# Kernel optimization log

Measured on AMD Instinct MI355X. Metric: run time of the kernel, lower is better.

Reference implementation:

```python
import jax, jax.numpy as jnp
import numpy as np

NEG_SLOPE = 0.2
EPS = 1e-16

def gat_conv(x, edge_index, W, a_src, a_dst, b):
    # x: [N, Fin], W: [Fin, C], a_src/a_dst: [C], b: [C]
    N = x.shape[0]
    src, dst = edge_index[0], edge_index[1]
    h = x @ W                                  # [N, C]
    alpha_s = h @ a_src                        # [N]
    alpha_d = h @ a_dst                        # [N]
    e = alpha_s[src] + alpha_d[dst]            # [E]
    e = jnp.where(e > 0, e, NEG_SLOPE * e)     # LeakyReLU(0.2)
    # ragged softmax over incoming edges of each dst node
    m = jax.ops.segment_max(e, dst, num_segments=N)       # [N]
    p = jnp.exp(e - m[dst])                                # [E]
    s = jax.ops.segment_sum(p, dst, num_segments=N)        # [N]
    alpha = p / (s[dst] + EPS)                             # [E]
    out = jax.ops.segment_sum(alpha[:, None] * h[src], dst, num_segments=N)
    return out + b

def setup_inputs() -> dict:
    key = jax.random.key(0)
    ks = jax.random.split(key, 10)
    N, Fin, H, C, E = 50000, 128, 64, 64, 800000
    x = jax.random.normal(ks[0], (N, Fin), dtype=jnp.float32)
    edge_index = jax.random.randint(ks[1], (2, E), 0, N, dtype=jnp.int64)
    sc1 = 1.0 / np.sqrt(Fin)
    sc2 = 1.0 / np.sqrt(H)
    W1 = jax.random.normal(ks[2], (Fin, H), dtype=jnp.float32) * sc1
    a_src1 = jax.random.normal(ks[3], (H,), dtype=jnp.float32) * sc2
    a_dst1 = jax.random.normal(ks[4], (H,), dtype=jnp.float32) * sc2
    b1 = jnp.zeros((H,), dtype=jnp.float32)
    W2 = jax.random.normal(ks[5], (H, C), dtype=jnp.float32) * sc2
    a_src2 = jax.random.normal(ks[6], (C,), dtype=jnp.float32) * sc2
    a_dst2 = jax.random.normal(ks[7], (C,), dtype=jnp.float32) * sc2
    b2 = jnp.zeros((C,), dtype=jnp.float32)
    return {"x": x, "edge_index": edge_index, "W1": W1, "a_src1": a_src1,
            "a_dst1": a_dst1, "b1": b1, "W2": W2, "a_src2": a_src2,
            "a_dst2": a_dst2, "b2": b2}

def reference(x, edge_index, W1, a_src1, a_dst1, b1, W2, a_src2, a_dst2, b2):
    h = gat_conv(x, edge_index, W1, a_src1, a_dst1, b1)
    h = jax.nn.relu(h)
    out = gat_conv(h, edge_index, W2, a_src2, a_dst2, b2)
    return out
```

## Files before the change

kernel.cpp:

```cpp
#include <hip/hip_runtime.h>
#include <cstddef>

constexpr int FIN = 128;
constexpr int EPB = 2048;
constexpr int BSH = 7;
constexpr int NPB = 128;
constexpr int PACK_SH = 25;

typedef _Float16 half4 __attribute__((ext_vector_type(4)));
typedef _Float16 half8 __attribute__((ext_vector_type(8)));
typedef float floatx4 __attribute__((ext_vector_type(4)));

__device__ __forceinline__ int block_scan_tot(int v, int tid, int* wsums,
                                              int* tot) {
    int lane = tid & 63, w = tid >> 6;
    int x = v;
#pragma unroll
    for (int off = 1; off < 64; off <<= 1) {
        int y = __shfl_up(x, off, 64);
        if (lane >= off) x += y;
    }
    if (lane == 63) wsums[w] = x;
    __syncthreads();
    int add = 0;
#pragma unroll
    for (int i = 0; i < 4; ++i) add += (i < w) ? wsums[i] : 0;
    *tot = wsums[0] + wsums[1] + wsums[2] + wsums[3];
    return x + add - v;
}

template <int K, typename XT>
__device__ __forceinline__
void gemm_mfma_body(const XT* __restrict__ X, const float* __restrict__ W,
                    const float* __restrict__ ASRC, const float* __restrict__ ADST,
                    _Float16* __restrict__ Hh, float* __restrict__ AS,
                    float* __restrict__ AD, int N, int blk,
                    _Float16* Xh, _Float16* WT) {
    constexpr int LDH = K + 8;
    const int tid = threadIdx.x;
    const int nb = blk * 64;

    if constexpr (sizeof(XT) == 4) {
        constexpr int QPR = K / 4;
        for (int i = tid; i < 64 * QPR; i += 256) {
            int r = i / QPR, q = i % QPR;
            float4 v = make_float4(0.f, 0.f, 0.f, 0.f);
            if (nb + r < N) v = *(const float4*)(X + (size_t)(nb + r) * K + 4 * q);
            half4 h; h[0] = (_Float16)v.x; h[1] = (_Float16)v.y;
            h[2] = (_Float16)v.z; h[3] = (_Float16)v.w;
            *(half4*)(Xh + r * LDH + 4 * q) = h;
        }
    } else {
        constexpr int OPR = K / 8;
        for (int i = tid; i < 64 * OPR; i += 256) {
            int r = i / OPR, o = i % OPR;
            half8 v = {};
            if (nb + r < N) v = *(const half8*)(X + (size_t)(nb + r) * K + 8 * o);
            *(half8*)(Xh + r * LDH + 8 * o) = v;
        }
    }
    for (int i = tid; i < 64 * (K / 4); i += 256) {
        int n = i & 63, kg = i >> 6;
        half4 h;
#pragma unroll
        for (int j = 0; j < 4; ++j)
            h[j] = (_Float16)W[(4 * kg + j) * 64 + n];
        *(half4*)(WT + n * LDH + 4 * kg) = h;
    }
    __syncthreads();

    const int l = tid & 63;
    const int r0 = (tid >> 6) * 16;
    const int n16 = l & 15, quad = l >> 4;

    floatx4 acc[4];
#pragma unroll
    for (int nt = 0; nt < 4; ++nt) acc[nt] = (floatx4){0.f, 0.f, 0.f, 0.f};

#pragma unroll
    for (int k0 = 0; k0 < K; k0 += 32) {
        half8 a = *(const half8*)(Xh + (r0 + n16) * LDH + k0 + quad * 8);
#pragma unroll
        for (int nt = 0; nt < 4; ++nt) {
            half8 b = *(const half8*)(WT + (nt * 16 + n16) * LDH + k0 + quad * 8);
            acc[nt] = __builtin_amdgcn_mfma_f32_16x16x32_f16(a, b, acc[nt], 0, 0, 0);
        }
    }

    float pa[4] = {0.f, 0.f, 0.f, 0.f}, pd[4] = {0.f, 0.f, 0.f, 0.f};
#pragma unroll
    for (int nt = 0; nt < 4; ++nt) {
        float as_v = ASRC[nt * 16 + n16], ad_v = ADST[nt * 16 + n16];
#pragma unroll
        for (int reg = 0; reg < 4; ++reg) {
            pa[reg] += acc[nt][reg] * as_v;
            pd[reg] += acc[nt][reg] * ad_v;
        }
    }
#pragma unroll
    for (int off = 1; off < 16; off <<= 1) {
#pragma unroll
        for (int reg = 0; reg < 4; ++reg) {
            pa[reg] += __shfl_xor(pa[reg], off, 64);
            pd[reg] += __shfl_xor(pd[reg], off, 64);
        }
    }
    if (n16 == 0) {
#pragma unroll
        for (int reg = 0; reg < 4; ++reg) {
            int row = nb + r0 + quad * 4 + reg;
            if (row < N) { AS[row] = pa[reg]; AD[row] = pd[reg]; }
        }
    }

#pragma unroll
    for (int nt = 0; nt < 4; ++nt)
#pragma unroll
        for (int reg = 0; reg < 4; ++reg)
            Xh[(r0 + quad * 4 + reg) * LDH + nt * 16 + n16] = (_Float16)acc[nt][reg];
    {
        int r = r0 + (l >> 2);
        int o = (l & 3) * 16;
        if (nb + r < N) {
            half8 v0 = *(const half8*)(Xh + r * LDH + o);
            half8 v1 = *(const half8*)(Xh + r * LDH + o + 8);
            *(half8*)(Hh + (size_t)(nb + r) * 64 + o) = v0;
            *(half8*)(Hh + (size_t)(nb + r) * 64 + o + 8) = v1;
        }
    }
}

__global__ __launch_bounds__(256)
void gemm1_and_count(const float* __restrict__ X, const float* __restrict__ W,
                     const float* __restrict__ ASRC, const float* __restrict__ ADST,
                     _Float16* __restrict__ Hh, float* __restrict__ AS,
                     float* __restrict__ AD, int N,
                     const int* __restrict__ dst, int E, int nblk, int nbuck,
                     int* __restrict__ cnts, int* __restrict__ ticket) {
    constexpr int K = FIN, LDH = K + 8;
    __shared__ _Float16 Xh[64 * LDH];
    __shared__ _Float16 WT[64 * LDH];

    const int tid = threadIdx.x;
    if ((int)blockIdx.x < nblk) {
        int* hist = (int*)Xh;
        if (blockIdx.x == 0 && tid == 0) *ticket = 0;
        for (int i = tid; i < nbuck; i += 256) hist[i] = 0;
        __syncthreads();
        int e0 = blockIdx.x * EPB;
        int e1 = min(e0 + EPB, E);
        for (int e = e0 + tid; e < e1; e += 256)
            atomicAdd(&hist[dst[e] >> BSH], 1);
        __syncthreads();
        for (int i = tid; i < nbuck; i += 256)
            cnts[blockIdx.x * nbuck + i] = hist[i];
        return;
    }
    gemm_mfma_body<K, float>(X, W, ASRC, ADST, Hh, AS, AD, N,
                             blockIdx.x - nblk, Xh, WT);
}

template <int K, typename XT>
__global__ __launch_bounds__(256)
void gemm_feat(const XT* __restrict__ X, const float* __restrict__ W,
               const float* __restrict__ ASRC, const float* __restrict__ ADST,
               _Float16* __restrict__ Hh, float* __restrict__ AS,
               float* __restrict__ AD, int N) {
    constexpr int LDH = K + 8;
    __shared__ _Float16 Xh[64 * LDH];
    __shared__ _Float16 WT[64 * LDH];
    gemm_mfma_body<K, XT>(X, W, ASRC, ADST, Hh, AS, AD, N, blockIdx.x, Xh, WT);
}

__global__ __launch_bounds__(256)
void bucket_colscan_fused(int* __restrict__ cnts, int nblk, int nbuck,
                          int* __restrict__ btotal, int* __restrict__ bbase,
                          int* __restrict__ ticket) {
    __shared__ int wsums[4];
    __shared__ int lastflag;
    int b = blockIdx.x;
    int tid = threadIdx.x;
    int carry = 0;
    for (int c0 = 0; c0 < nblk; c0 += 256) {
        int t = c0 + tid;
        int v = (t < nblk) ? cnts[t * nbuck + b] : 0;
        int tot;
        int e = block_scan_tot(v, tid, wsums, &tot);
        if (t < nblk) cnts[t * nbuck + b] = e + carry;
        carry += tot;
        __syncthreads();
    }
    if (tid == 0) {
        atomicExch(&btotal[b], carry);
        int old = atomicAdd(ticket, 1);
        lastflag = (old == nbuck - 1);
    }
    __syncthreads();
    if (!lastflag) return;
    int i0 = 2 * tid, i1 = 2 * tid + 1;
    int v0 = (i0 < nbuck) ? atomicAdd(&btotal[i0], 0) : 0;
    int v1 = (i1 < nbuck) ? atomicAdd(&btotal[i1], 0) : 0;
    __syncthreads();
    int tot2;
    int e2 = block_scan_tot(v0 + v1, tid, wsums, &tot2);
    if (i0 <= nbuck) bbase[i0] = e2;
    if (i1 <= nbuck) bbase[i1] = e2 + v0;
}

__global__ __launch_bounds__(256)
void bucket_scatter(const int* __restrict__ src, const int* __restrict__ dst,
                    int E, int nbuck, const int* __restrict__ cnts,
                    const int* __restrict__ bbase, int* __restrict__ ebuck) {
    __shared__ int cur[512];
    int tid = threadIdx.x;
    for (int i = tid; i < nbuck; i += 256)
        cur[i] = bbase[i] + cnts[blockIdx.x * nbuck + i];
    __syncthreads();
    int e0 = blockIdx.x * EPB;
    int e1 = min(e0 + EPB, E);
    for (int e = e0 + tid; e < e1; e += 256) {
        int d = dst[e];
        int p = atomicAdd(&cur[d >> BSH], 1);
        ebuck[p] = ((d & (NPB - 1)) << PACK_SH) | src[e];
    }
}

__global__ __launch_bounds__(256)
void bucket_to_csr(const int* __restrict__ ebuck, const int* __restrict__ bbase,
                   int N, int E, int* __restrict__ row_ptr,
                   int* __restrict__ csr_src) {
    __shared__ int hist[NPB];
    __shared__ int cur[NPB];
    __shared__ int wsums[4];
    int b = blockIdx.x, tid = threadIdx.x;
    int nstart = b << BSH;
    int base = bbase[b], endp = bbase[b + 1];
    if (tid < NPB) hist[tid] = 0;
    __syncthreads();
    for (int e = base + tid; e < endp; e += 256)
        atomicAdd(&hist[((unsigned)ebuck[e]) >> PACK_SH], 1);
    __syncthreads();
    int v = (tid < NPB) ? hist[tid] : 0;
    int tot;
    int excl = block_scan_tot(v, tid, wsums, &tot);
    if (tid < NPB) {
        cur[tid] = excl;
        if (nstart + tid < N) row_ptr[nstart + tid] = base + excl;
    }
    if (b == 0 && tid == 0) row_ptr[N] = E;
    __syncthreads();
    for (int e = base + tid; e < endp; e += 256) {
        int pv = ebuck[e];
        int p = atomicAdd(&cur[((unsigned)pv) >> PACK_SH], 1);
        csr_src[base + p] = pv & ((1 << PACK_SH) - 1);
    }
}

template <typename OT>
__device__ __forceinline__
void agg_one_node(const _Float16* __restrict__ Hh, const float* __restrict__ AS,
                  const float* __restrict__ AD, const int* __restrict__ csr_src,
                  const float* __restrict__ bias, OT* __restrict__ OUT,
                  int n, int base, int end, int lane, int relu) {
    const int cnt = end - base;
    const float adn = AD[n];

    if (cnt > 64) {
        float m = -INFINITY;
        for (int c0 = base; c0 < end; c0 += 64) {
            int c = min(64, end - c0);
            float e = -INFINITY;
            if (lane < c) {
                int sr = csr_src[c0 + lane];
                float t = AS[sr] + adn;
                e = t > 0.f ? t : 0.2f * t;
            }
#pragma unroll
            for (int off = 32; off > 0; off >>= 1) e = fmaxf(e, __shfl_xor(e, off, 64));
            m = fmaxf(m, e);
        }
        float s = 0.f, acc = 0.f;
        for (int c0 = base; c0 < end; c0 += 64) {
            int c = min(64, end - c0);
            int srcl = 0;
            float p = 0.f;
            if (lane < c) {
                srcl = csr_src[c0 + lane];
                float t = AS[srcl] + adn;
                t = t > 0.f ? t : 0.2f * t;
                p = __expf(t - m);
            }
            float cs = p;
#pragma unroll
            for (int off = 32; off > 0; off >>= 1) cs += __shfl_xor(cs, off, 64);
            s += cs;
            for (int j = 0; j < c; ++j)
                acc += __shfl(p, j, 64) *
                       (float)Hh[(size_t)__shfl(srcl, j, 64) * 64 + lane];
        }
        float o = acc * (1.f / (s + 1e-16f)) + bias[lane];
        if (relu) o = fmaxf(o, 0.f);
        OUT[(size_t)n * 64 + lane] = (OT)o;
        return;
    }

    int srcl = 0;
    float el = 0.f;
    if (lane < cnt) {
        srcl = csr_src[base + lane];
        float e = AS[srcl] + adn;
        el = e > 0.f ? e : 0.2f * e;
    }
    float p = (lane < cnt) ? __expf(el) : 0.f;
    float s = p;
#pragma unroll
    for (int off = 32; off > 0; off >>= 1) s += __shfl_xor(s, off, 64);
    const float inv = 1.f / (s + 1e-16f);

    const int eg = lane >> 3;
    const int c8 = (lane & 7) * 8;

    float acc[8], acc2[8];
#pragma unroll
    for (int t = 0; t < 8; ++t) { acc[t] = 0.f; acc2[t] = 0.f; }

    int j = 0;
    for (; j + 16 <= cnt; j += 16) {
        int iA = j + eg, iB = j + 8 + eg;
        int sA = __shfl(srcl, iA, 64), sB = __shfl(srcl, iB, 64);
        float aA = __shfl(p, iA, 64),  aB = __shfl(p, iB, 64);
        half8 hA = *(const half8*)(Hh + (size_t)sA * 64 + c8);
        half8 hB = *(const half8*)(Hh + (size_t)sB * 64 + c8);
#pragma unroll
        for (int t = 0; t < 8; ++t) {
            acc[t]  += aA * (float)hA[t];
            acc2[t] += aB * (float)hB[t];
        }
    }
    for (; j < cnt; j += 8) {
        int iA = j + eg;
        int sA = __shfl(srcl, iA, 64);
        float aA = __shfl(p, iA, 64);
        half8 hA = *(const half8*)(Hh + (size_t)sA * 64 + c8);
#pragma unroll
        for (int t = 0; t < 8; ++t) acc[t] += aA * (float)hA[t];
    }
#pragma unroll
    for (int t = 0; t < 8; ++t) acc[t] += acc2[t];
#pragma unroll
    for (int off = 8; off <= 32; off <<= 1)
#pragma unroll
        for (int t = 0; t < 8; ++t) acc[t] += __shfl_xor(acc[t], off, 64);

    if (lane < 8) {
        float4 b0 = *(const float4*)(bias + c8);
        float4 b1 = *(const float4*)(bias + c8 + 4);
        float o[8];
        o[0] = acc[0] * inv + b0.x; o[1] = acc[1] * inv + b0.y;
        o[2] = acc[2] * inv + b0.z; o[3] = acc[3] * inv + b0.w;
        o[4] = acc[4] * inv + b1.x; o[5] = acc[5] * inv + b1.y;
        o[6] = acc[6] * inv + b1.z; o[7] = acc[7] * inv + b1.w;
        if (relu) {
#pragma unroll
            for (int t = 0; t < 8; ++t) o[t] = fmaxf(o[t], 0.f);
        }
        if constexpr (sizeof(OT) == 2) {
            half8 hv;
#pragma unroll
            for (int t = 0; t < 8; ++t) hv[t] = (_Float16)o[t];
            *(half8*)((_Float16*)OUT + (size_t)n * 64 + c8) = hv;
        } else {
            *(float4*)((float*)OUT + (size_t)n * 64 + c8) =
                make_float4(o[0], o[1], o[2], o[3]);
            *(float4*)((float*)OUT + (size_t)n * 64 + c8 + 4) =
                make_float4(o[4], o[5], o[6], o[7]);
        }
    }
}

template <typename OT>
__global__ __launch_bounds__(256)
void gat_aggregate(const _Float16* __restrict__ Hh, const float* __restrict__ AS,
                   const float* __restrict__ AD, const int* __restrict__ row_ptr,
                   const int* __restrict__ csr_src, const float* __restrict__ bias,
                   OT* __restrict__ OUT, int N, int relu) {
    const int lane = threadIdx.x & 63;
    const int half = lane >> 5;
    const int l32  = lane & 31;
    const int pair0 = blockIdx.x * 8 + (threadIdx.x >> 6) * 2;
    if (pair0 >= N) return;
    const int n = pair0 + half;

    int base = 0, end = 0;
    if (n < N) { base = row_ptr[n]; end = row_ptr[n + 1]; }
    const int cnt = end - base;

    if (!__all(cnt <= 32)) {
        int baseA = __shfl(base, 0, 64),  endA = __shfl(end, 0, 64);
        int baseB = __shfl(base, 32, 64), endB = __shfl(end, 32, 64);
        agg_one_node(Hh, AS, AD, csr_src, bias, OUT, pair0, baseA, endA, lane, relu);
        if (pair0 + 1 < N)
            agg_one_node(Hh, AS, AD, csr_src, bias, OUT, pair0 + 1, baseB, endB,
                         lane, relu);
        return;
    }

    const float adn = (n < N) ? AD[n] : 0.f;
    int srcl = 0;
    float p = 0.f;
    if (l32 < cnt) {
        srcl = csr_src[base + l32];
        float e = AS[srcl] + adn;
        e = e > 0.f ? e : 0.2f * e;
        p = __expf(e);
    }
    float s = p;
#pragma unroll
    for (int off = 16; off > 0; off >>= 1) s += __shfl_xor(s, off, 64);
    const float inv = 1.f / (s + 1e-16f);

    const int eg = l32 >> 3;
    const int c8 = (l32 & 7) * 8;

    float acc[8], acc2[8];
#pragma unroll
    for (int t = 0; t < 8; ++t) { acc[t] = 0.f; acc2[t] = 0.f; }

    int j = 0;
    for (; j + 8 <= cnt; j += 8) {
        int iA = j + eg, iB = j + 4 + eg;
        int sA = __shfl(srcl, iA, 32), sB = __shfl(srcl, iB, 32);
        float aA = __shfl(p, iA, 32),  aB = __shfl(p, iB, 32);
        half8 hA = *(const half8*)(Hh + (size_t)sA * 64 + c8);
        half8 hB = *(const half8*)(Hh + (size_t)sB * 64 + c8);
#pragma unroll
        for (int t = 0; t < 8; ++t) {
            acc[t]  += aA * (float)hA[t];
            acc2[t] += aB * (float)hB[t];
        }
    }
    for (; j < cnt; j += 4) {
        int iA = j + eg;
        int sA = __shfl(srcl, iA, 32);
        float aA = __shfl(p, iA, 32);
        half8 hA = *(const half8*)(Hh + (size_t)sA * 64 + c8);
#pragma unroll
        for (int t = 0; t < 8; ++t) acc[t] += aA * (float)hA[t];
    }
#pragma unroll
    for (int t = 0; t < 8; ++t) acc[t] += acc2[t];
#pragma unroll
    for (int t = 0; t < 8; ++t) acc[t] += __shfl_xor(acc[t], 8, 64);
#pragma unroll
    for (int t = 0; t < 8; ++t) acc[t] += __shfl_xor(acc[t], 16, 64);

    if (l32 < 8 && n < N) {
        float4 b0 = *(const float4*)(bias + c8);
        float4 b1 = *(const float4*)(bias + c8 + 4);
        float o[8];
        o[0] = acc[0] * inv + b0.x; o[1] = acc[1] * inv + b0.y;
        o[2] = acc[2] * inv + b0.z; o[3] = acc[3] * inv + b0.w;
        o[4] = acc[4] * inv + b1.x; o[5] = acc[5] * inv + b1.y;
        o[6] = acc[6] * inv + b1.z; o[7] = acc[7] * inv + b1.w;
        if (relu) {
#pragma unroll
            for (int t = 0; t < 8; ++t) o[t] = fmaxf(o[t], 0.f);
        }
        if constexpr (sizeof(OT) == 2) {
            half8 hv;
#pragma unroll
            for (int t = 0; t < 8; ++t) hv[t] = (_Float16)o[t];
            *(half8*)((_Float16*)OUT + (size_t)n * 64 + c8) = hv;
        } else {
            *(float4*)((float*)OUT + (size_t)n * 64 + c8) =
                make_float4(o[0], o[1], o[2], o[3]);
            *(float4*)((float*)OUT + (size_t)n * 64 + c8 + 4) =
                make_float4(o[4], o[5], o[6], o[7]);
        }
    }
}

extern "C" void kernel_launch(void* const* d_in, const int* in_sizes, int n_in,
                              void* d_out, int out_size, void* d_ws, size_t ws_size,
                              hipStream_t stream) {
    const float* x    = (const float*)d_in[0];
    const int*   ei   = (const int*)d_in[1];
    const float* W1   = (const float*)d_in[2];
    const float* as1w = (const float*)d_in[3];
    const float* ad1w = (const float*)d_in[4];
    const float* b1   = (const float*)d_in[5];
    const float* W2   = (const float*)d_in[6];
    const float* as2w = (const float*)d_in[7];
    const float* ad2w = (const float*)d_in[8];
    const float* b2   = (const float*)d_in[9];
    float* out = (float*)d_out;

    const int N = in_sizes[0] / FIN;
    const int E = in_sizes[1] / 2;
    const int* esrc = ei;
    const int* edst = ei + E;

    const int nbuck = (N + NPB - 1) >> BSH;
    const int nblk  = (E + EPB - 1) / EPB;

    char* wp8 = (char*)d_ws;
    _Float16* Hh  = (_Float16*)wp8;  wp8 += (size_t)N * 64 * 2;
    _Float16* R1h = (_Float16*)wp8;  wp8 += (size_t)N * 64 * 2;
    float* AS1 = (float*)wp8;        wp8 += (size_t)N * 4;
    float* AD1 = (float*)wp8;        wp8 += (size_t)N * 4;
    float* AS2 = (float*)wp8;        wp8 += (size_t)N * 4;
    float* AD2 = (float*)wp8;        wp8 += (size_t)N * 4;
    int* row_ptr = (int*)wp8;        wp8 += (size_t)(N + 1) * 4;
    int* csr     = (int*)wp8;        wp8 += (size_t)E * 4;
    int* ebuck   = (int*)wp8;        wp8 += (size_t)E * 4;
    int* cnts    = (int*)wp8;        wp8 += (size_t)nblk * nbuck * 4;
    int* btotal  = (int*)wp8;        wp8 += (size_t)nbuck * 4;
    int* bbase   = (int*)wp8;        wp8 += (size_t)(nbuck + 1) * 4;
    int* ticket  = (int*)wp8;        wp8 += 4;

    const int nbG = (N + 63) / 64;
    const int nbAgg = (N + 7) / 8;

    hipLaunchKernelGGL(gemm1_and_count, dim3(nblk + nbG), dim3(256), 0, stream,
                       x, W1, as1w, ad1w, Hh, AS1, AD1, N,
                       edst, E, nblk, nbuck, cnts, ticket);
    hipLaunchKernelGGL(bucket_colscan_fused, dim3(nbuck), dim3(256), 0, stream,
                       cnts, nblk, nbuck, btotal, bbase, ticket);
    hipLaunchKernelGGL(bucket_scatter, dim3(nblk), dim3(256), 0, stream,
                       esrc, edst, E, nbuck, cnts, bbase, ebuck);
    hipLaunchKernelGGL(bucket_to_csr, dim3(nbuck), dim3(256), 0, stream,
                       ebuck, bbase, N, E, row_ptr, csr);
    hipLaunchKernelGGL(gat_aggregate<_Float16>, dim3(nbAgg), dim3(256), 0,
                       stream, Hh, AS1, AD1, row_ptr, csr, b1, R1h, N, 1);
    hipLaunchKernelGGL((gemm_feat<64, _Float16>), dim3(nbG), dim3(256), 0, stream,
                       R1h, W2, as2w, ad2w, Hh, AS2, AD2, N);
    hipLaunchKernelGGL(gat_aggregate<float>, dim3(nbAgg), dim3(256), 0,
                       stream, Hh, AS2, AD2, row_ptr, csr, b2, out, N, 0);
}
```

Before: 174.7 us.

## Build CSR via per-node degree atomics instead of two-pass bucket sort

Replaces the bucketed counting sort (per-block bucket histograms, column scan, bucket scatter, then per-bucket CSR build) with a direct global per-node degree count, a per-bucket scan of degrees, and a single scatter using per-node global atomic cursors. This removes one kernel launch and the intermediate packed edge buffer pass, and adds a memset. The cost moves to 800k global atomics on degree and cursor arrays, and the edge order within each row becomes nondeterministic, which may change floating-point sums and locality.

```diff
diff --git a/kernel.cpp b/kernel.cpp
--- a/kernel.cpp
+++ b/kernel.cpp
@@ -5,7 +5,6 @@
 constexpr int EPB = 2048;
 constexpr int BSH = 7;
 constexpr int NPB = 128;
-constexpr int PACK_SH = 25;
 
 typedef _Float16 half4 __attribute__((ext_vector_type(4)));
 typedef _Float16 half8 __attribute__((ext_vector_type(8)));
@@ -135,25 +134,19 @@
                      const float* __restrict__ ASRC, const float* __restrict__ ADST,
                      _Float16* __restrict__ Hh, float* __restrict__ AS,
                      float* __restrict__ AD, int N,
-                     const int* __restrict__ dst, int E, int nblk, int nbuck,
-                     int* __restrict__ cnts, int* __restrict__ ticket) {
+                     const int* __restrict__ dst, int E, int nblk,
+                     int* __restrict__ degree, int* __restrict__ ticket) {
     constexpr int K = FIN, LDH = K + 8;
     __shared__ _Float16 Xh[64 * LDH];
     __shared__ _Float16 WT[64 * LDH];
 
     const int tid = threadIdx.x;
     if ((int)blockIdx.x < nblk) {
-        int* hist = (int*)Xh;
         if (blockIdx.x == 0 && tid == 0) *ticket = 0;
-        for (int i = tid; i < nbuck; i += 256) hist[i] = 0;
-        __syncthreads();
         int e0 = blockIdx.x * EPB;
         int e1 = min(e0 + EPB, E);
         for (int e = e0 + tid; e < e1; e += 256)
-            atomicAdd(&hist[dst[e] >> BSH], 1);
-        __syncthreads();
-        for (int i = tid; i < nbuck; i += 256)
-            cnts[blockIdx.x * nbuck + i] = hist[i];
+            atomicAdd(&degree[dst[e]], 1);
         return;
     }
     gemm_mfma_body<K, float>(X, W, ASRC, ADST, Hh, AS, AD, N,
@@ -173,25 +166,21 @@
 }
 
 __global__ __launch_bounds__(256)
-void bucket_colscan_fused(int* __restrict__ cnts, int nblk, int nbuck,
-                          int* __restrict__ btotal, int* __restrict__ bbase,
-                          int* __restrict__ ticket) {
+void degree_scan(const int* __restrict__ degree, int N, int nbuck,
+                 int* __restrict__ rel, int* __restrict__ cursor,
+                 int* __restrict__ btotal, int* __restrict__ bbase,
+                 int* __restrict__ ticket) {
     __shared__ int wsums[4];
     __shared__ int lastflag;
-    int b = blockIdx.x;
-    int tid = threadIdx.x;
-    int carry = 0;
-    for (int c0 = 0; c0 < nblk; c0 += 256) {
-        int t = c0 + tid;
-        int v = (t < nblk) ? cnts[t * nbuck + b] : 0;
-        int tot;
-        int e = block_scan_tot(v, tid, wsums, &tot);
-        if (t < nblk) cnts[t * nbuck + b] = e + carry;
-        carry += tot;
-        __syncthreads();
-    }
+    int b = blockIdx.x, tid = threadIdx.x;
+    int n = (b << BSH) + tid;
+    int v = (tid < NPB && n < N) ? degree[n] : 0;
+    int tot;
+    int e = block_scan_tot(v, tid, wsums, &tot);
+    if (tid < NPB && n < N) { rel[n] = e; cursor[n] = e; }
+    __syncthreads();
     if (tid == 0) {
-        atomicExch(&btotal[b], carry);
+        atomicExch(&btotal[b], tot);
         int old = atomicAdd(ticket, 1);
         lastflag = (old == nbuck - 1);
     }
@@ -208,51 +197,20 @@
 }
 
 __global__ __launch_bounds__(256)
-void bucket_scatter(const int* __restrict__ src, const int* __restrict__ dst,
-                    int E, int nbuck, const int* __restrict__ cnts,
-                    const int* __restrict__ bbase, int* __restrict__ ebuck) {
-    __shared__ int cur[512];
+void scatter_csr(const int* __restrict__ src, const int* __restrict__ dst,
+                 int E, int N, const int* __restrict__ bbase,
+                 const int* __restrict__ rel, int* __restrict__ cursor,
+                 int* __restrict__ row_ptr, int* __restrict__ csr_src) {
     int tid = threadIdx.x;
-    for (int i = tid; i < nbuck; i += 256)
-        cur[i] = bbase[i] + cnts[blockIdx.x * nbuck + i];
-    __syncthreads();
+    for (int n = blockIdx.x * 256 + tid; n < N; n += gridDim.x * 256)
+        row_ptr[n] = bbase[n >> BSH] + rel[n];
+    if (blockIdx.x == 0 && tid == 0) row_ptr[N] = E;
     int e0 = blockIdx.x * EPB;
     int e1 = min(e0 + EPB, E);
     for (int e = e0 + tid; e < e1; e += 256) {
         int d = dst[e];
-        int p = atomicAdd(&cur[d >> BSH], 1);
-        ebuck[p] = ((d & (NPB - 1)) << PACK_SH) | src[e];
-    }
-}
-
-__global__ __launch_bounds__(256)
-void bucket_to_csr(const int* __restrict__ ebuck, const int* __restrict__ bbase,
-                   int N, int E, int* __restrict__ row_ptr,
-                   int* __restrict__ csr_src) {
-    __shared__ int hist[NPB];
-    __shared__ int cur[NPB];
-    __shared__ int wsums[4];
-    int b = blockIdx.x, tid = threadIdx.x;
-    int nstart = b << BSH;
-    int base = bbase[b], endp = bbase[b + 1];
-    if (tid < NPB) hist[tid] = 0;
-    __syncthreads();
-    for (int e = base + tid; e < endp; e += 256)
-        atomicAdd(&hist[((unsigned)ebuck[e]) >> PACK_SH], 1);
-    __syncthreads();
-    int v = (tid < NPB) ? hist[tid] : 0;
-    int tot;
-    int excl = block_scan_tot(v, tid, wsums, &tot);
-    if (tid < NPB) {
-        cur[tid] = excl;
-        if (nstart + tid < N) row_ptr[nstart + tid] = base + excl;
-    }
-    if (b == 0 && tid == 0) row_ptr[N] = E;
-    __syncthreads();
-    for (int e = base + tid; e < endp; e += 256) {
-        int pv = ebuck[e];
-        int p = atomicAdd(&cur[((unsigned)pv) >> PACK_SH], 1);
-        csr_src[base + p] = pv & ((1 << PACK_SH) - 1);
+        int p = bbase[d >> BSH] + atomicAdd(&cursor[d], 1);
+        csr_src[p] = src[e];
     }
 }
 
@@ -512,8 +470,9 @@
     float* AD2 = (float*)wp8;        wp8 += (size_t)N * 4;
     int* row_ptr = (int*)wp8;        wp8 += (size_t)(N + 1) * 4;
     int* csr     = (int*)wp8;        wp8 += (size_t)E * 4;
-    int* ebuck   = (int*)wp8;        wp8 += (size_t)E * 4;
-    int* cnts    = (int*)wp8;        wp8 += (size_t)nblk * nbuck * 4;
+    int* degree  = (int*)wp8;        wp8 += (size_t)N * 4;
+    int* rel     = (int*)wp8;        wp8 += (size_t)N * 4;
+    int* cursor  = (int*)wp8;        wp8 += (size_t)N * 4;
     int* btotal  = (int*)wp8;        wp8 += (size_t)nbuck * 4;
     int* bbase   = (int*)wp8;        wp8 += (size_t)(nbuck + 1) * 4;
     int* ticket  = (int*)wp8;        wp8 += 4;
@@ -521,15 +480,14 @@
     const int nbG = (N + 63) / 64;
     const int nbAgg = (N + 7) / 8;
 
+    hipMemsetAsync(degree, 0, (size_t)N * 4, stream);
     hipLaunchKernelGGL(gemm1_and_count, dim3(nblk + nbG), dim3(256), 0, stream,
                        x, W1, as1w, ad1w, Hh, AS1, AD1, N,
-                       edst, E, nblk, nbuck, cnts, ticket);
-    hipLaunchKernelGGL(bucket_colscan_fused, dim3(nbuck), dim3(256), 0, stream,
-                       cnts, nblk, nbuck, btotal, bbase, ticket);
-    hipLaunchKernelGGL(bucket_scatter, dim3(nblk), dim3(256), 0, stream,
-                       esrc, edst, E, nbuck, cnts, bbase, ebuck);
-    hipLaunchKernelGGL(bucket_to_csr, dim3(nbuck), dim3(256), 0, stream,
-                       ebuck, bbase, N, E, row_ptr, csr);
+                       edst, E, nblk, degree, ticket);
+    hipLaunchKernelGGL(degree_scan, dim3(nbuck), dim3(256), 0, stream,
+                       degree, N, nbuck, rel, cursor, btotal, bbase, ticket);
+    hipLaunchKernelGGL(scatter_csr, dim3(nblk), dim3(256), 0, stream,
+                       esrc, edst, E, N, bbase, rel, cursor, row_ptr, csr);
     hipLaunchKernelGGL(gat_aggregate<_Float16>, dim3(nbAgg), dim3(256), 0,
                        stream, Hh, AS1, AD1, row_ptr, csr, b1, R1h, N, 1);
     hipLaunchKernelGGL((gemm_feat<64, _Float16>), dim3(nbG), dim3(256), 0, stream,
```

Measured after the change: 230.9 us. +32.2%, slower.

## Sort edges locally in the count pass and gather buckets in LDS

Applied to the files above, without the earlier changes.

The histogram pass in the GEMM1 kernel now also sorts each 2048-edge chunk by bucket in shared memory. It writes the sorted chunk contiguously, along with per-block bucket row offsets. The separate bucket_scatter kernel and its scattered global atomic writes are removed. bucket_to_csr now gathers each bucket's runs from every chunk into an LDS buffer before the per-node counting sort. This saves a launch and a pass of random global writes, but adds more shared-memory use per block, serial per-thread gather loops, and a fixed LDS cap. Buckets larger than that cap would silently lose edges.

```diff
diff --git a/kernel.cpp b/kernel.cpp
--- a/kernel.cpp
+++ b/kernel.cpp
@@ -6,6 +6,8 @@
 constexpr int BSH = 7;
 constexpr int NPB = 128;
 constexpr int PACK_SH = 25;
+constexpr int RSTR = 512;
+constexpr int CAP = 4608;
 
 typedef _Float16 half4 __attribute__((ext_vector_type(4)));
 typedef _Float16 half8 __attribute__((ext_vector_type(8)));
@@ -131,29 +133,74 @@
 }
 
 __global__ __launch_bounds__(256)
-void gemm1_and_count(const float* __restrict__ X, const float* __restrict__ W,
-                     const float* __restrict__ ASRC, const float* __restrict__ ADST,
-                     _Float16* __restrict__ Hh, float* __restrict__ AS,
-                     float* __restrict__ AD, int N,
-                     const int* __restrict__ dst, int E, int nblk, int nbuck,
-                     int* __restrict__ cnts, int* __restrict__ ticket) {
+void gemm1_and_sort(const float* __restrict__ X, const float* __restrict__ W,
+                    const float* __restrict__ ASRC, const float* __restrict__ ADST,
+                    _Float16* __restrict__ Hh, float* __restrict__ AS,
+                    float* __restrict__ AD, int N,
+                    const int* __restrict__ src, const int* __restrict__ dst,
+                    int E, int nblk, int nbuck,
+                    int* __restrict__ cnts, int* __restrict__ rows,
+                    int* __restrict__ ebuck, int* __restrict__ ticket) {
     constexpr int K = FIN, LDH = K + 8;
     __shared__ _Float16 Xh[64 * LDH];
     __shared__ _Float16 WT[64 * LDH];
+    __shared__ int wsums[4];
 
     const int tid = threadIdx.x;
     if ((int)blockIdx.x < nblk) {
-        int* hist = (int*)Xh;
+        int* sorted = (int*)Xh;
+        int* hist   = (int*)WT;
+        int* cur    = hist + 512;
         if (blockIdx.x == 0 && tid == 0) *ticket = 0;
         for (int i = tid; i < nbuck; i += 256) hist[i] = 0;
         __syncthreads();
-        int e0 = blockIdx.x * EPB;
-        int e1 = min(e0 + EPB, E);
-        for (int e = e0 + tid; e < e1; e += 256)
-            atomicAdd(&hist[dst[e] >> BSH], 1);
+
+        const int e0 = blockIdx.x * EPB;
+        const int e1 = min(e0 + EPB, E);
+        const int cnt = e1 - e0;
+
+        int pay[8], bk[8];
+#pragma unroll
+        for (int k = 0; k < 8; ++k) {
+            int e = e0 + tid + k * 256;
+            bk[k] = -1; pay[k] = 0;
+            if (e < e1) {
+                int d = dst[e];
+                bk[k] = d >> BSH;
+                pay[k] = ((d & (NPB - 1)) << PACK_SH) | src[e];
+                atomicAdd(&hist[bk[k]], 1);
+            }
+        }
         __syncthreads();
-        for (int i = tid; i < nbuck; i += 256)
-            cnts[blockIdx.x * nbuck + i] = hist[i];
+
+        int i0 = 2 * tid, i1 = 2 * tid + 1;
+        int v0 = (i0 < nbuck) ? hist[i0] : 0;
+        int v1 = (i1 < nbuck) ? hist[i1] : 0;
+        int tot;
+        int ex = block_scan_tot(v0 + v1, tid, wsums, &tot);
+        if (i0 < nbuck) {
+            cur[i0] = ex;
+            rows[blockIdx.x * RSTR + i0] = ex;
+            cnts[blockIdx.x * nbuck + i0] = v0;
+        }
+        if (i1 < nbuck) {
+            cur[i1] = ex + v0;
+            rows[blockIdx.x * RSTR + i1] = ex + v0;
+            cnts[blockIdx.x * nbuck + i1] = v1;
+        }
+        if (tid == 0) rows[blockIdx.x * RSTR + nbuck] = cnt;
+        __syncthreads();
+
+#pragma unroll
+        for (int k = 0; k < 8; ++k) {
+            if (bk[k] >= 0) {
+                int p = atomicAdd(&cur[bk[k]], 1);
+                sorted[p] = pay[k];
+            }
+        }
+        __syncthreads();
+        for (int i = tid; i < cnt; i += 256)
+            ebuck[blockIdx.x * EPB + i] = sorted[i];
         return;
     }
     gemm_mfma_body<K, float>(X, W, ASRC, ADST, Hh, AS, AD, N,
@@ -208,37 +255,33 @@
 }
 
 __global__ __launch_bounds__(256)
-void bucket_scatter(const int* __restrict__ src, const int* __restrict__ dst,
-                    int E, int nbuck, const int* __restrict__ cnts,
-                    const int* __restrict__ bbase, int* __restrict__ ebuck) {
-    __shared__ int cur[512];
-    int tid = threadIdx.x;
-    for (int i = tid; i < nbuck; i += 256)
-        cur[i] = bbase[i] + cnts[blockIdx.x * nbuck + i];
-    __syncthreads();
-    int e0 = blockIdx.x * EPB;
-    int e1 = min(e0 + EPB, E);
-    for (int e = e0 + tid; e < e1; e += 256) {
-        int d = dst[e];
-        int p = atomicAdd(&cur[d >> BSH], 1);
-        ebuck[p] = ((d & (NPB - 1)) << PACK_SH) | src[e];
-    }
-}
-
-__global__ __launch_bounds__(256)
-void bucket_to_csr(const int* __restrict__ ebuck, const int* __restrict__ bbase,
-                   int N, int E, int* __restrict__ row_ptr,
-                   int* __restrict__ csr_src) {
+void bucket_to_csr(const int* __restrict__ ebuck, const int* __restrict__ rows,
+                   const int* __restrict__ cnts, const int* __restrict__ bbase,
+                   int N, int E, int nblk, int nbuck,
+                   int* __restrict__ row_ptr, int* __restrict__ csr_src) {
+    __shared__ int eL[CAP];
     __shared__ int hist[NPB];
     __shared__ int cur[NPB];
     __shared__ int wsums[4];
-    int b = blockIdx.x, tid = threadIdx.x;
-    int nstart = b << BSH;
-    int base = bbase[b], endp = bbase[b + 1];
+    const int b = blockIdx.x, tid = threadIdx.x;
+    const int nstart = b << BSH;
+    const int base = bbase[b], endp = bbase[b + 1];
+    const int btot = endp - base;
+
     if (tid < NPB) hist[tid] = 0;
-    __syncthreads();
-    for (int e = base + tid; e < endp; e += 256)
-        atomicAdd(&hist[((unsigned)ebuck[e]) >> PACK_SH], 1);
+    for (int blk = tid; blk < nblk; blk += 256) {
+        int r0 = rows[blk * RSTR + b];
+        int r1 = rows[blk * RSTR + b + 1];
+        int c0 = cnts[blk * nbuck + b];
+        for (int i = 0; i < r1 - r0; ++i) {
+            int c = c0 + i;
+            if (c < CAP) eL[c] = ebuck[blk * EPB + r0 + i];
+        }
+    }
+    __syncthreads();
+
+    for (int e = tid; e < btot; e += 256)
+        atomicAdd(&hist[((unsigned)eL[e]) >> PACK_SH], 1);
     __syncthreads();
     int v = (tid < NPB) ? hist[tid] : 0;
     int tot;
@@ -249,8 +292,8 @@
     }
     if (b == 0 && tid == 0) row_ptr[N] = E;
     __syncthreads();
-    for (int e = base + tid; e < endp; e += 256) {
-        int pv = ebuck[e];
+    for (int e = tid; e < btot; e += 256) {
+        int pv = eL[e];
         int p = atomicAdd(&cur[((unsigned)pv) >> PACK_SH], 1);
         csr_src[base + p] = pv & ((1 << PACK_SH) - 1);
     }
@@ -512,8 +555,9 @@
     float* AD2 = (float*)wp8;        wp8 += (size_t)N * 4;
     int* row_ptr = (int*)wp8;        wp8 += (size_t)(N + 1) * 4;
     int* csr     = (int*)wp8;        wp8 += (size_t)E * 4;
-    int* ebuck   = (int*)wp8;        wp8 += (size_t)E * 4;
+    int* ebuck   = (int*)wp8;        wp8 += (size_t)nblk * EPB * 4;
     int* cnts    = (int*)wp8;        wp8 += (size_t)nblk * nbuck * 4;
+    int* rows    = (int*)wp8;        wp8 += (size_t)nblk * RSTR * 4;
     int* btotal  = (int*)wp8;        wp8 += (size_t)nbuck * 4;
     int* bbase   = (int*)wp8;        wp8 += (size_t)(nbuck + 1) * 4;
     int* ticket  = (int*)wp8;        wp8 += 4;
@@ -521,15 +565,13 @@
     const int nbG = (N + 63) / 64;
     const int nbAgg = (N + 7) / 8;
 
-    hipLaunchKernelGGL(gemm1_and_count, dim3(nblk + nbG), dim3(256), 0, stream,
+    hipLaunchKernelGGL(gemm1_and_sort, dim3(nblk + nbG), dim3(256), 0, stream,
                        x, W1, as1w, ad1w, Hh, AS1, AD1, N,
-                       edst, E, nblk, nbuck, cnts, ticket);
+                       esrc, edst, E, nblk, nbuck, cnts, rows, ebuck, ticket);
     hipLaunchKernelGGL(bucket_colscan_fused, dim3(nbuck), dim3(256), 0, stream,
                        cnts, nblk, nbuck, btotal, bbase, ticket);
-    hipLaunchKernelGGL(bucket_scatter, dim3(nblk), dim3(256), 0, stream,
-                       esrc, edst, E, nbuck, cnts, bbase, ebuck);
     hipLaunchKernelGGL(bucket_to_csr, dim3(nbuck), dim3(256), 0, stream,
-                       ebuck, bbase, N, E, row_ptr, csr);
+                       ebuck, rows, cnts, bbase, N, E, nblk, nbuck, row_ptr, csr);
     hipLaunchKernelGGL(gat_aggregate<_Float16>, dim3(nbAgg), dim3(256), 0,
                        stream, Hh, AS1, AD1, row_ptr, csr, b1, R1h, N, 1);
     hipLaunchKernelGGL((gemm_feat<64, _Float16>), dim3(nbG), dim3(256), 0, stream,
```

New measurement: 174.8 us. Within noise of the previous version (+0.1%).
